# Kernel tuning notes

Hardware: AMD Instinct MI355X
Metric: run time of the kernel (lower is better)

## Reference

```python
import jax, jax.numpy as jnp
import numpy as np

H, D, RPE_DIM, LAYERS = 8, 64, 64, 3
GAMMA = 0.999  # fixed decay (use_decay=True, requires_grad=False)
EPS = 1e-8

def simple_rmsnorm(x):
    # SimpleRMSNorm: x / (||x||_2 * d^{-1/2} + eps), no learned scale
    rms = jnp.sqrt(jnp.sum(x * x, axis=-1, keepdims=True)) * (x.shape[-1] ** -0.5)
    return x / (rms + EPS)

def rpe_transform(idx, pos_proj_w, pos_proj_b, layer_ws, layer_bs, out_w, out_b):
    # idx: (n, 1) -> (H, n, D)
    x = idx @ pos_proj_w + pos_proj_b            # (n, RPE_DIM)
    for i in range(LAYERS):                       # residual=False -> sequential
        x = jax.nn.relu(simple_rmsnorm(x)) @ layer_ws[i] + layer_bs[i]
    x = jax.nn.relu(simple_rmsnorm(x)) @ out_w + out_b   # (n, H*D)
    n = x.shape[0]
    return x.reshape(n, H, D).transpose(1, 0, 2)  # (H, n, D)

def setup_inputs() -> dict:
    key = jax.random.key(0)
    ks = jax.random.split(key, 6)
    b, n = 8, 4096
    s = RPE_DIM ** -0.5
    return {
        "x": jax.random.normal(ks[0], (b, H, n, D), jnp.float32),
        "pos_proj_w": jax.random.normal(ks[1], (1, RPE_DIM), jnp.float32),
        "pos_proj_b": jnp.zeros((RPE_DIM,), jnp.float32),
        "layer_ws": jax.random.normal(ks[2], (LAYERS, RPE_DIM, RPE_DIM), jnp.float32) * s,
        "layer_bs": jnp.zeros((LAYERS, RPE_DIM), jnp.float32),
        "out_w": jax.random.normal(ks[3], (RPE_DIM, H * D), jnp.float32) * s,
        "out_b": jnp.zeros((H * D,), jnp.float32),
    }

def reference(x, pos_proj_w, pos_proj_b, layer_ws, layer_bs, out_w, out_b):
    b, h, n, d = x.shape
    _rpe = lambda idx: rpe_transform(idx, pos_proj_w, pos_proj_b, layer_ws, layer_bs, out_w, out_b)
    # relative-position kernel values (par_type=1: raw integer offsets)
    zero = _rpe(jnp.zeros((1, 1), x.dtype))                       # (H, 1, D)
    pos_idx = jnp.arange(1, n, dtype=x.dtype).reshape(n - 1, 1)   # 1..n-1
    pos = _rpe(pos_idx)                                           # (H, n-1, D)
    neg = _rpe(-pos_idx[::-1])                                    # -(n-1)..-1
    # fixed exponential decay gamma^|offset|
    coef = jnp.arange(1, n, dtype=x.dtype).reshape(1, n - 1, 1)
    gamma = jnp.full((h, 1, d), GAMMA, x.dtype) ** coef           # (H, n-1, D)
    pos = gamma * pos
    neg = gamma[:, ::-1, :] * neg
    # act_type='none' -> identity activation on a
    a = jnp.concatenate([zero, pos, zero, neg], axis=1)           # (H, 2n, D)
    # circular conv of length 2n realizes the Toeplitz matvec
    y = jnp.fft.rfft(x, n=2 * n, axis=-2)                         # (b,H,n+1?,D) complex
    v = jnp.fft.rfft(a, n=2 * n, axis=-2)[None]                   # (1,H,.,D)
    out = jnp.fft.irfft(v * y, n=2 * n, axis=-2)[:, :, :n, :]
    return out
```

## Files before the change

### kernel.cpp

```cpp
#include <hip/hip_runtime.h>
#include <math.h>

#define NF 8192

__device__ __forceinline__ int phys(int e) { return e ^ (((e >> 4) & 7) << 1); }

__device__ __forceinline__ float2 cmul(float2 a, float2 b) {
    return make_float2(a.x*b.x - a.y*b.y, a.x*b.y + a.y*b.x);
}
__device__ __forceinline__ float2 cmulc(float2 a, float2 b) {
    return make_float2(a.x*b.x + a.y*b.y, a.y*b.x - a.x*b.y);
}
__device__ __forceinline__ float2 cadd(float2 a, float2 b){ return make_float2(a.x+b.x, a.y+b.y); }
__device__ __forceinline__ float2 csub(float2 a, float2 b){ return make_float2(a.x-b.x, a.y-b.y); }
__device__ __forceinline__ float2 mnegi(float2 a){ return make_float2(a.y, -a.x); }
__device__ __forceinline__ float2 mposi(float2 a){ return make_float2(-a.y, a.x); }
#define RSQ2 0.70710678118654752f
__device__ __forceinline__ float2 mw81 (float2 a){ return make_float2( RSQ2*(a.x+a.y),  RSQ2*(a.y-a.x)); }
__device__ __forceinline__ float2 mw83 (float2 a){ return make_float2( RSQ2*(a.y-a.x), -RSQ2*(a.x+a.y)); }
__device__ __forceinline__ float2 mw81c(float2 a){ return make_float2( RSQ2*(a.x-a.y),  RSQ2*(a.x+a.y)); }
__device__ __forceinline__ float2 mw83c(float2 a){ return make_float2(-RSQ2*(a.x+a.y),  RSQ2*(a.x-a.y)); }

#define C16_1 0.92387953251128674f
#define S16_1 0.38268343236508978f
#define C16_2 0.70710678118654752f

__device__ __forceinline__ float2 twbase(int ts) {
    float fa = (float)ts * (1.0f/8192.0f);
    return make_float2(__builtin_amdgcn_cosf(fa), -__builtin_amdgcn_sinf(fa));
}

__device__ __forceinline__ void dif8_core(float2& v0, float2& v1, float2& v2, float2& v3,
                                          float2& v4, float2& v5, float2& v6, float2& v7) {
    float2 t;
    t = csub(v0, v4); v0 = cadd(v0, v4); v4 = t;
    t = csub(v1, v5); v1 = cadd(v1, v5); v5 = mw81(t);
    t = csub(v2, v6); v2 = cadd(v2, v6); v6 = mnegi(t);
    t = csub(v3, v7); v3 = cadd(v3, v7); v7 = mw83(t);
    t = csub(v0, v2); v0 = cadd(v0, v2); v2 = t;
    t = csub(v1, v3); v1 = cadd(v1, v3); v3 = mnegi(t);
    t = csub(v4, v6); v4 = cadd(v4, v6); v6 = t;
    t = csub(v5, v7); v5 = cadd(v5, v7); v7 = mnegi(t);
    t = csub(v0, v1); v0 = cadd(v0, v1); v1 = t;
    t = csub(v2, v3); v2 = cadd(v2, v3); v3 = t;
    t = csub(v4, v5); v4 = cadd(v4, v5); v5 = t;
    t = csub(v6, v7); v6 = cadd(v6, v7); v7 = t;
}

__device__ __forceinline__ void dit8_core(float2& v0, float2& v1, float2& v2, float2& v3,
                                          float2& v4, float2& v5, float2& v6, float2& v7) {
    float2 t;
    t = csub(v0, v1); v0 = cadd(v0, v1); v1 = t;
    t = csub(v2, v3); v2 = cadd(v2, v3); v3 = t;
    t = csub(v4, v5); v4 = cadd(v4, v5); v5 = t;
    t = csub(v6, v7); v6 = cadd(v6, v7); v7 = t;
    t = v2;        v2 = csub(v0, t); v0 = cadd(v0, t);
    t = mposi(v3); v3 = csub(v1, t); v1 = cadd(v1, t);
    t = v6;        v6 = csub(v4, t); v4 = cadd(v4, t);
    t = mposi(v7); v7 = csub(v5, t); v5 = cadd(v5, t);
    t = v4;        v4 = csub(v0, t); v0 = cadd(v0, t);
    t = mw81c(v5); v5 = csub(v1, t); v1 = cadd(v1, t);
    t = mposi(v6); v6 = csub(v2, t); v2 = cadd(v2, t);
    t = mw83c(v7); v7 = csub(v3, t); v3 = cadd(v3, t);
}

#define TW_POWERS(ts) \
    float2 w1 = twbase(ts); \
    float2 w2 = cmul(w1, w1); \
    float2 w3 = cmul(w2, w1); \
    float2 w4 = cmul(w2, w2); \
    float2 w5 = cmul(w3, w2); \
    float2 w6 = cmul(w3, w3); \
    float2 w7 = cmul(w4, w3);

template<int M, int LM>
__device__ __forceinline__ void fwd8_lds(float2* Z, int tid) {
    #pragma unroll
    for (int q = 0; q < 2; ++q) {
        int beta = tid + q*512;
        int i    = beta & (M-1);
        int base = ((beta >> LM) << (LM+3)) + i;
        float2 v0 = Z[phys(base        )];
        float2 v1 = Z[phys(base + 1*M)];
        float2 v2 = Z[phys(base + 2*M)];
        float2 v3 = Z[phys(base + 3*M)];
        float2 v4 = Z[phys(base + 4*M)];
        float2 v5 = Z[phys(base + 5*M)];
        float2 v6 = Z[phys(base + 6*M)];
        float2 v7 = Z[phys(base + 7*M)];
        dif8_core(v0,v1,v2,v3,v4,v5,v6,v7);
        TW_POWERS((NF >> (LM+3)) * i)
        Z[phys(base        )] = v0;
        Z[phys(base + 4*M)] = cmul(v1, w4);
        Z[phys(base + 2*M)] = cmul(v2, w2);
        Z[phys(base + 6*M)] = cmul(v3, w6);
        Z[phys(base + 1*M)] = cmul(v4, w1);
        Z[phys(base + 5*M)] = cmul(v5, w5);
        Z[phys(base + 3*M)] = cmul(v6, w3);
        Z[phys(base + 7*M)] = cmul(v7, w7);
    }
}

template<int M, int LM>
__device__ __forceinline__ void inv8_lds(float2* Z, int tid) {
    #pragma unroll
    for (int q = 0; q < 2; ++q) {
        int beta = tid + q*512;
        int i    = beta & (M-1);
        int base = ((beta >> LM) << (LM+3)) + i;
        TW_POWERS((NF >> (LM+3)) * i)
        float2 v0 = Z[phys(base        )];
        float2 v1 = cmulc(Z[phys(base + 4*M)], w4);
        float2 v2 = cmulc(Z[phys(base + 2*M)], w2);
        float2 v3 = cmulc(Z[phys(base + 6*M)], w6);
        float2 v4 = cmulc(Z[phys(base + 1*M)], w1);
        float2 v5 = cmulc(Z[phys(base + 5*M)], w5);
        float2 v6 = cmulc(Z[phys(base + 3*M)], w3);
        float2 v7 = cmulc(Z[phys(base + 7*M)], w7);
        dit8_core(v0,v1,v2,v3,v4,v5,v6,v7);
        Z[phys(base        )] = v0;
        Z[phys(base + 1*M)] = v1;
        Z[phys(base + 2*M)] = v2;
        Z[phys(base + 3*M)] = v3;
        Z[phys(base + 4*M)] = v4;
        Z[phys(base + 5*M)] = v5;
        Z[phys(base + 6*M)] = v6;
        Z[phys(base + 7*M)] = v7;
    }
}

__device__ __forceinline__ void fft8192_conv(float2* Z, int tid, const float4* __restrict__ A4,
                                             const float2 (&vin)[8], float2 (&vout)[8])
{
    #pragma unroll
    for (int q = 0; q < 2; ++q) {
        int i = tid + q*512;
        float2 v0 = vin[q*4+0];
        float2 v1 = vin[q*4+1];
        float2 v2 = vin[q*4+2];
        float2 v3 = vin[q*4+3];
        float2 v4 = v0;
        float2 v5 = mw81(v1);
        float2 v6 = mnegi(v2);
        float2 v7 = mw83(v3);
        float2 t;
        t = csub(v0, v2); v0 = cadd(v0, v2); v2 = t;
        t = csub(v1, v3); v1 = cadd(v1, v3); v3 = mnegi(t);
        t = csub(v4, v6); v4 = cadd(v4, v6); v6 = t;
        t = csub(v5, v7); v5 = cadd(v5, v7); v7 = mnegi(t);
        t = csub(v0, v1); v0 = cadd(v0, v1); v1 = t;
        t = csub(v2, v3); v2 = cadd(v2, v3); v3 = t;
        t = csub(v4, v5); v4 = cadd(v4, v5); v5 = t;
        t = csub(v6, v7); v6 = cadd(v6, v7); v7 = t;
        TW_POWERS(i)
        Z[phys(i        )] = v0;
        Z[phys(i + 4096)] = cmul(v1, w4);
        Z[phys(i + 2048)] = cmul(v2, w2);
        Z[phys(i + 6144)] = cmul(v3, w6);
        Z[phys(i + 1024)] = cmul(v4, w1);
        Z[phys(i + 5120)] = cmul(v5, w5);
        Z[phys(i + 3072)] = cmul(v6, w3);
        Z[phys(i + 7168)] = cmul(v7, w7);
    }
    __syncthreads();
    fwd8_lds<128, 7>(Z, tid);  __syncthreads();
    fwd8_lds<16,  4>(Z, tid);  __syncthreads();

    {
        int c = tid, sw4 = c & 7;
        float4* Z4 = reinterpret_cast<float4*>(Z);
        float2 z[16];
        #pragma unroll
        for (int j = 0; j < 8; ++j) {
            float4 wv = Z4[c*8 + (j ^ sw4)];
            z[2*j]   = make_float2(wv.x, wv.y);
            z[2*j+1] = make_float2(wv.z, wv.w);
        }
        dif8_core(z[0],z[2],z[4],z[6],z[8],z[10],z[12],z[14]);
        dif8_core(z[1],z[3],z[5],z[7],z[9],z[11],z[13],z[15]);
        #define P4K(k, ZE, ZO, WR, WI) { \
            float2 w = make_float2((WR)*(ZO).x - (WI)*(ZO).y, (WR)*(ZO).y + (WI)*(ZO).x); \
            float2 pp = cadd(ZE, w), rr = csub(ZE, w); \
            float4 av = A4[(k)*512 + c]; \
            pp = cmul(pp, make_float2(av.x, av.y)); \
            rr = cmul(rr, make_float2(av.z, av.w)); \
            ZE = cadd(pp, rr); \
            ZO = csub(pp, rr); }
        { float2 pp = cadd(z[0], z[1]), rr = csub(z[0], z[1]);
          float4 av = A4[0*512 + c];
          pp = cmul(pp, make_float2(av.x, av.y));
          rr = cmul(rr, make_float2(av.z, av.w));
          z[0] = cadd(pp, rr); z[1] = csub(pp, rr); }
        P4K(1, z[8],  z[9],   C16_1, -S16_1)
        P4K(2, z[4],  z[5],   C16_2, -C16_2)
        P4K(3, z[12], z[13],  S16_1, -C16_1)
        { float2 w = mnegi(z[3]);
          float2 pp = cadd(z[2], w), rr = csub(z[2], w);
          float4 av = A4[4*512 + c];
          pp = cmul(pp, make_float2(av.x, av.y));
          rr = cmul(rr, make_float2(av.z, av.w));
          z[2] = cadd(pp, rr); z[3] = csub(pp, rr); }
        P4K(5, z[10], z[11], -S16_1, -C16_1)
        P4K(6, z[6],  z[7],  -C16_2, -C16_2)
        P4K(7, z[14], z[15], -C16_1, -S16_1)
        #undef P4K
        z[3]  = mposi(z[3]);
        z[5]  = cmul(z[5],  make_float2( C16_2,  C16_2));
        z[7]  = cmul(z[7],  make_float2(-C16_2,  C16_2));
        z[9]  = cmul(z[9],  make_float2( C16_1,  S16_1));
        z[11] = cmul(z[11], make_float2(-S16_1,  C16_1));
        z[13] = cmul(z[13], make_float2( S16_1,  C16_1));
        z[15] = cmul(z[15], make_float2(-C16_1,  S16_1));
        dit8_core(z[0],z[2],z[4],z[6],z[8],z[10],z[12],z[14]);
        dit8_core(z[1],z[3],z[5],z[7],z[9],z[11],z[13],z[15]);
        #pragma unroll
        for (int j = 0; j < 8; ++j)
            Z4[c*8 + (j ^ sw4)] = make_float4(z[2*j].x, z[2*j].y, z[2*j+1].x, z[2*j+1].y);
    }
    __syncthreads();
    inv8_lds<16,  4>(Z, tid);  __syncthreads();
    inv8_lds<128, 7>(Z, tid);  __syncthreads();

    #pragma unroll
    for (int q = 0; q < 2; ++q) {
        int i = tid + q*512;
        TW_POWERS(i)
        float2 v0 = Z[phys(i        )];
        float2 v1 = cmulc(Z[phys(i + 4096)], w4);
        float2 v2 = cmulc(Z[phys(i + 2048)], w2);
        float2 v3 = cmulc(Z[phys(i + 6144)], w6);
        float2 v4 = cmulc(Z[phys(i + 1024)], w1);
        float2 v5 = cmulc(Z[phys(i + 5120)], w5);
        float2 v6 = cmulc(Z[phys(i + 3072)], w3);
        float2 v7 = cmulc(Z[phys(i + 7168)], w7);
        float2 t;
        t = csub(v0, v1); v0 = cadd(v0, v1); v1 = t;
        t = csub(v2, v3); v2 = cadd(v2, v3); v3 = t;
        t = csub(v4, v5); v4 = cadd(v4, v5); v5 = t;
        t = csub(v6, v7); v6 = cadd(v6, v7); v7 = t;
        t = v2;        v2 = csub(v0, t); v0 = cadd(v0, t);
        t = mposi(v3); v3 = csub(v1, t); v1 = cadd(v1, t);
        t = v6;        v6 = csub(v4, t); v4 = cadd(v4, t);
        t = mposi(v7); v7 = csub(v5, t); v5 = cadd(v5, t);
        vout[q*4+0] = cadd(v0, v4);
        vout[q*4+1] = cadd(v1, mw81c(v5));
        vout[q*4+2] = cadd(v2, mposi(v6));
        vout[q*4+3] = cadd(v3, mw83c(v7));
    }
}


__global__ __launch_bounds__(512) void rpe_kernel(
    const float* __restrict__ pw,  const float* __restrict__ pb,
    const float* __restrict__ lws, const float* __restrict__ lbs,
    const float* __restrict__ ow,  const float* __restrict__ ob,
    float* __restrict__ a_buf)
{
    __shared__ float sW2[3][32][64][2];
    __shared__ float sWo2[32][64][2];
    __shared__ float sB[3][64];
    __shared__ float sPW[64], sPB[64];
    __shared__ float sAct[8][2][64];
    int tid = threadIdx.x;
    for (int idx = tid; idx < 3*64*64; idx += 512) {
        int L = idx >> 12, rem = idx & 4095, k = rem >> 6, c = rem & 63;
        sW2[L][k >> 1][c][k & 1] = lws[idx];
    }
    if (tid < 192) ((float*)sB)[tid] = lbs[tid];
    if (tid < 64) { sPW[tid] = pw[tid]; sPB[tid] = pb[tid]; }
    __syncthreads();

    int wv = tid >> 6, lane = tid & 63;
    int e0 = blockIdx.x * 16 + wv * 2;
    float xv[2], dec[2];
    #pragma unroll
    for (int s = 0; s < 2; ++s) {
        int e = e0 + s;
        float p = (e == 4096) ? 0.f : ((e < 4096) ? (float)e : (float)(e - 8192));
        int m = (e < 4096) ? e : (8192 - e);
        if (e == 4096) m = 0;
        dec[s] = exp2f(-0.0014434309482562475f * (float)m);
        xv[s] = fmaf(p, sPW[lane], sPB[lane]);
    }

    #pragma unroll
    for (int L = 0; L < 3; ++L) {
        #pragma unroll
        for (int s = 0; s < 2; ++s) {
            float v = xv[s];
            float ss = v * v;
            #pragma unroll
            for (int o = 1; o < 64; o <<= 1) ss += __shfl_xor(ss, o);
            sAct[wv][s][lane] = fmaxf(v / (sqrtf(ss) * 0.125f + 1e-8f), 0.f);
            float y = sB[L][lane];
            const float2* ap = reinterpret_cast<const float2*>(sAct[wv][s]);
            const float2* wp = reinterpret_cast<const float2*>(sW2[L]);
            #pragma unroll
            for (int kk = 0; kk < 32; ++kk) {
                float2 a2 = ap[kk];
                float2 ww = wp[kk*64 + lane];
                y = fmaf(a2.x, ww.x, y);
                y = fmaf(a2.y, ww.y, y);
            }
            xv[s] = y;
        }
    }
    #pragma unroll
    for (int s = 0; s < 2; ++s) {
        float v = xv[s];
        float ss = v * v;
        #pragma unroll
        for (int o = 1; o < 64; o <<= 1) ss += __shfl_xor(ss, o);
        sAct[wv][s][lane] = fmaxf(v / (sqrtf(ss) * 0.125f + 1e-8f), 0.f);
    }
    for (int qq = 0; qq < 8; ++qq) {
        __syncthreads();
        for (int idx = tid; idx < 4096; idx += 512) {
            int k = idx >> 6, c = idx & 63;
            sWo2[k >> 1][c][k & 1] = ow[(size_t)k*512 + qq*64 + c];
        }
        __syncthreads();
        #pragma unroll
        for (int s = 0; s < 2; ++s) {
            float y = ob[qq*64 + lane];
            const float2* ap = reinterpret_cast<const float2*>(sAct[wv][s]);
            const float2* wp = reinterpret_cast<const float2*>(sWo2);
            #pragma unroll
            for (int kk = 0; kk < 32; ++kk) {
                float2 a2 = ap[kk];
                float2 ww = wp[kk*64 + lane];
                y = fmaf(a2.x, ww.x, y);
                y = fmaf(a2.y, ww.y, y);
            }
            a_buf[(size_t)(qq*64 + lane)*NF + (e0 + s)] = y * dec[s];
        }
    }
}

__global__ __launch_bounds__(512, 4) void afft_kernel(
    const float* __restrict__ a_buf, float2* __restrict__ Afft)
{
    __shared__ __align__(16) float2 Z[NF];
    int cc = blockIdx.x, tid = threadIdx.x;
    const float* col = a_buf + (size_t)cc * NF;
    #pragma unroll
    for (int q = 0; q < 2; ++q) {
        int i = tid + q*512;
        float2 v0 = make_float2(col[i       ], 0.f);
        float2 v1 = make_float2(col[i + 1024], 0.f);
        float2 v2 = make_float2(col[i + 2048], 0.f);
        float2 v3 = make_float2(col[i + 3072], 0.f);
        float2 v4 = make_float2(col[i + 4096], 0.f);
        float2 v5 = make_float2(col[i + 5120], 0.f);
        float2 v6 = make_float2(col[i + 6144], 0.f);
        float2 v7 = make_float2(col[i + 7168], 0.f);
        dif8_core(v0,v1,v2,v3,v4,v5,v6,v7);
        TW_POWERS(i)
        Z[phys(i        )] = v0;
        Z[phys(i + 4096)] = cmul(v1, w4);
        Z[phys(i + 2048)] = cmul(v2, w2);
        Z[phys(i + 6144)] = cmul(v3, w6);
        Z[phys(i + 1024)] = cmul(v4, w1);
        Z[phys(i + 5120)] = cmul(v5, w5);
        Z[phys(i + 3072)] = cmul(v6, w3);
        Z[phys(i + 7168)] = cmul(v7, w7);
    }
    __syncthreads();
    fwd8_lds<128, 7>(Z, tid);  __syncthreads();
    fwd8_lds<16,  4>(Z, tid);  __syncthreads();
    {
        int c = tid, sw4 = c & 7;
        float4* Z4 = reinterpret_cast<float4*>(Z);
        float4* oc4 = reinterpret_cast<float4*>(Afft + (size_t)cc * NF);
        float2 z[16];
        #pragma unroll
        for (int j = 0; j < 8; ++j) {
            float4 wv = Z4[c*8 + (j ^ sw4)];
            z[2*j]   = make_float2(wv.x, wv.y);
            z[2*j+1] = make_float2(wv.z, wv.w);
        }
        dif8_core(z[0],z[2],z[4],z[6],z[8],z[10],z[12],z[14]);
        dif8_core(z[1],z[3],z[5],z[7],z[9],z[11],z[13],z[15]);
        #define A4K(k, ZE, ZO, WR, WI) { \
            float2 w = make_float2((WR)*(ZO).x - (WI)*(ZO).y, (WR)*(ZO).y + (WI)*(ZO).x); \
            float2 pp = cadd(ZE, w), rr = csub(ZE, w); \
            oc4[(k)*512 + c] = make_float4(pp.x, pp.y, rr.x, rr.y); }
        { float2 pp = cadd(z[0], z[1]), rr = csub(z[0], z[1]);
          oc4[0*512 + c] = make_float4(pp.x, pp.y, rr.x, rr.y); }
        A4K(1, z[8],  z[9],   C16_1, -S16_1)
        A4K(2, z[4],  z[5],   C16_2, -C16_2)
        A4K(3, z[12], z[13],  S16_1, -C16_1)
        { float2 w = mnegi(z[3]);
          float2 pp = cadd(z[2], w), rr = csub(z[2], w);
          oc4[4*512 + c] = make_float4(pp.x, pp.y, rr.x, rr.y); }
        A4K(5, z[10], z[11], -S16_1, -C16_1)
        A4K(6, z[6],  z[7],  -C16_2, -C16_2)
        A4K(7, z[14], z[15], -C16_1, -S16_1)
        #undef A4K
    }
}

__global__ __launch_bounds__(512, 4) void conv_kernel(
    const float* __restrict__ x, const float2* __restrict__ Afft,
    float* __restrict__ out)
{
    __shared__ __align__(16) float2 Z[NF];
    int blk = blockIdx.x;
    int c8 = blk & 7, r = blk >> 3;
    int dp = ((c8 & 1) << 4) | (r & 15);
    int h  = (((r >> 4) & 3) << 1) | ((c8 >> 1) & 1);
    int bp = (((r >> 6) & 1) << 1) | ((c8 >> 2) & 1);
    int d  = dp * 2;
    int tid = threadIdx.x;
    size_t base0 = ((size_t)((bp*2 + 0)*8 + h) * 4096) * 64 + d;
    size_t base1 = ((size_t)((bp*2 + 1)*8 + h) * 4096) * 64 + d;

    float2 inA[8], inB[8];
    #pragma unroll
    for (int q = 0; q < 2; ++q) {
        #pragma unroll
        for (int l = 0; l < 4; ++l) {
            int p = tid + q*512 + l*1024;
            float2 f0 = *reinterpret_cast<const float2*>(&x[base0 + (size_t)p*64]);
            float2 f1 = *reinterpret_cast<const float2*>(&x[base1 + (size_t)p*64]);
            inA[q*4+l] = make_float2(f0.x, f1.x);
            inB[q*4+l] = make_float2(f0.y, f1.y);
        }
    }

    const float4* A4a = reinterpret_cast<const float4*>(Afft + (size_t)(h*64 + d    )*NF);
    const float4* A4b = reinterpret_cast<const float4*>(Afft + (size_t)(h*64 + d + 1)*NF);
    float2 outA[8], outB[8];
    fft8192_conv(Z, tid, A4a, inA, outA);
    __syncthreads();
    fft8192_conv(Z, tid, A4b, inB, outB);

    const float sc = 1.0f/8192.0f;
    #pragma unroll
    for (int q = 0; q < 2; ++q) {
        #pragma unroll
        for (int l = 0; l < 4; ++l) {
            int p = tid + q*512 + l*1024;
            float2 yA = outA[q*4+l], yB = outB[q*4+l];
            *reinterpret_cast<float2*>(&out[base0 + (size_t)p*64]) = make_float2(yA.x * sc, yB.x * sc);
            *reinterpret_cast<float2*>(&out[base1 + (size_t)p*64]) = make_float2(yA.y * sc, yB.y * sc);
        }
    }
}

extern "C" void kernel_launch(void* const* d_in, const int* in_sizes, int n_in,
                              void* d_out, int out_size, void* d_ws, size_t ws_size,
                              hipStream_t stream) {
    const float* x   = (const float*)d_in[0];
    const float* pw  = (const float*)d_in[1];
    const float* pb  = (const float*)d_in[2];
    const float* lws = (const float*)d_in[3];
    const float* lbs = (const float*)d_in[4];
    const float* ow  = (const float*)d_in[5];
    const float* ob  = (const float*)d_in[6];
    float* out = (float*)d_out;
    char* ws = (char*)d_ws;
    float*  a_buf = (float*)ws;
    float2* Afft  = (float2*)(ws + (size_t)512*NF*4);

    rpe_kernel<<<512, 512, 0, stream>>>(pw, pb, lws, lbs, ow, ob, a_buf);
    afft_kernel<<<512, 512, 0, stream>>>(a_buf, Afft);
    conv_kernel<<<1024, 512, 0, stream>>>(x, Afft, out);
}
```

Baseline: 616.1 us.

## Pack two adjacent real channels into one complex FFT with Hermitian split

```diff
diff --git a/kernel.cpp b/kernel.cpp
--- a/kernel.cpp
+++ b/kernel.cpp
@@ -129,16 +129,177 @@
     }
 }
 
-__device__ __forceinline__ void fft8192_conv(float2* Z, int tid, const float4* __restrict__ A4,
-                                             const float2 (&vin)[8], float2 (&vout)[8])
+
+__global__ __launch_bounds__(512) void rpe_kernel(
+    const float* __restrict__ pw,  const float* __restrict__ pb,
+    const float* __restrict__ lws, const float* __restrict__ lbs,
+    const float* __restrict__ ow,  const float* __restrict__ ob,
+    float* __restrict__ a_buf)
 {
+    __shared__ float sW2[3][32][64][2];
+    __shared__ float sWo2[32][64][2];
+    __shared__ float sB[3][64];
+    __shared__ float sPW[64], sPB[64];
+    __shared__ float sAct[8][2][64];
+    int tid = threadIdx.x;
+    for (int idx = tid; idx < 3*64*64; idx += 512) {
+        int L = idx >> 12, rem = idx & 4095, k = rem >> 6, c = rem & 63;
+        sW2[L][k >> 1][c][k & 1] = lws[idx];
+    }
+    if (tid < 192) ((float*)sB)[tid] = lbs[tid];
+    if (tid < 64) { sPW[tid] = pw[tid]; sPB[tid] = pb[tid]; }
+    __syncthreads();
+
+    int wv = tid >> 6, lane = tid & 63;
+    int e0 = blockIdx.x * 16 + wv * 2;
+    float xv[2], dec[2];
+    #pragma unroll
+    for (int s = 0; s < 2; ++s) {
+        int e = e0 + s;
+        float p = (e == 4096) ? 0.f : ((e < 4096) ? (float)e : (float)(e - 8192));
+        int m = (e < 4096) ? e : (8192 - e);
+        if (e == 4096) m = 0;
+        dec[s] = exp2f(-0.0014434309482562475f * (float)m);
+        xv[s] = fmaf(p, sPW[lane], sPB[lane]);
+    }
+
+    #pragma unroll
+    for (int L = 0; L < 3; ++L) {
+        #pragma unroll
+        for (int s = 0; s < 2; ++s) {
+            float v = xv[s];
+            float ss = v * v;
+            #pragma unroll
+            for (int o = 1; o < 64; o <<= 1) ss += __shfl_xor(ss, o);
+            sAct[wv][s][lane] = fmaxf(v / (sqrtf(ss) * 0.125f + 1e-8f), 0.f);
+            float y = sB[L][lane];
+            const float2* ap = reinterpret_cast<const float2*>(sAct[wv][s]);
+            const float2* wp = reinterpret_cast<const float2*>(sW2[L]);
+            #pragma unroll
+            for (int kk = 0; kk < 32; ++kk) {
+                float2 a2 = ap[kk];
+                float2 ww = wp[kk*64 + lane];
+                y = fmaf(a2.x, ww.x, y);
+                y = fmaf(a2.y, ww.y, y);
+            }
+            xv[s] = y;
+        }
+    }
+    #pragma unroll
+    for (int s = 0; s < 2; ++s) {
+        float v = xv[s];
+        float ss = v * v;
+        #pragma unroll
+        for (int o = 1; o < 64; o <<= 1) ss += __shfl_xor(ss, o);
+        sAct[wv][s][lane] = fmaxf(v / (sqrtf(ss) * 0.125f + 1e-8f), 0.f);
+    }
+    for (int qq = 0; qq < 8; ++qq) {
+        __syncthreads();
+        for (int idx = tid; idx < 4096; idx += 512) {
+            int k = idx >> 6, c = idx & 63;
+            sWo2[k >> 1][c][k & 1] = ow[(size_t)k*512 + qq*64 + c];
+        }
+        __syncthreads();
+        #pragma unroll
+        for (int s = 0; s < 2; ++s) {
+            float y = ob[qq*64 + lane];
+            const float2* ap = reinterpret_cast<const float2*>(sAct[wv][s]);
+            const float2* wp = reinterpret_cast<const float2*>(sWo2);
+            #pragma unroll
+            for (int kk = 0; kk < 32; ++kk) {
+                float2 a2 = ap[kk];
+                float2 ww = wp[kk*64 + lane];
+                y = fmaf(a2.x, ww.x, y);
+                y = fmaf(a2.y, ww.y, y);
+            }
+            a_buf[(size_t)(qq*64 + lane)*NF + (e0 + s)] = y * dec[s];
+        }
+    }
+}
+
+__global__ __launch_bounds__(512, 4) void afft_kernel(
+    const float* __restrict__ a_buf, float2* __restrict__ Afft)
+{
+    __shared__ __align__(16) float2 Z[NF];
+    int cc = blockIdx.x, tid = threadIdx.x;
+    const float* col = a_buf + (size_t)cc * NF;
     #pragma unroll
     for (int q = 0; q < 2; ++q) {
         int i = tid + q*512;
-        float2 v0 = vin[q*4+0];
-        float2 v1 = vin[q*4+1];
-        float2 v2 = vin[q*4+2];
-        float2 v3 = vin[q*4+3];
+        float2 v0 = make_float2(col[i       ], 0.f);
+        float2 v1 = make_float2(col[i + 1024], 0.f);
+        float2 v2 = make_float2(col[i + 2048], 0.f);
+        float2 v3 = make_float2(col[i + 3072], 0.f);
+        float2 v4 = make_float2(col[i + 4096], 0.f);
+        float2 v5 = make_float2(col[i + 5120], 0.f);
+        float2 v6 = make_float2(col[i + 6144], 0.f);
+        float2 v7 = make_float2(col[i + 7168], 0.f);
+        dif8_core(v0,v1,v2,v3,v4,v5,v6,v7);
+        TW_POWERS(i)
+        Z[phys(i        )] = v0;
+        Z[phys(i + 4096)] = cmul(v1, w4);
+        Z[phys(i + 2048)] = cmul(v2, w2);
+        Z[phys(i + 6144)] = cmul(v3, w6);
+        Z[phys(i + 1024)] = cmul(v4, w1);
+        Z[phys(i + 5120)] = cmul(v5, w5);
+        Z[phys(i + 3072)] = cmul(v6, w3);
+        Z[phys(i + 7168)] = cmul(v7, w7);
+    }
+    __syncthreads();
+    fwd8_lds<128, 7>(Z, tid);  __syncthreads();
+    fwd8_lds<16,  4>(Z, tid);  __syncthreads();
+    {
+        int c = tid, sw4 = c & 7;
+        float4* Z4 = reinterpret_cast<float4*>(Z);
+        float4* oc4 = reinterpret_cast<float4*>(Afft + (size_t)cc * NF);
+        float2 z[16];
+        #pragma unroll
+        for (int j = 0; j < 8; ++j) {
+            float4 wv = Z4[c*8 + (j ^ sw4)];
+            z[2*j]   = make_float2(wv.x, wv.y);
+            z[2*j+1] = make_float2(wv.z, wv.w);
+        }
+        dif8_core(z[0],z[2],z[4],z[6],z[8],z[10],z[12],z[14]);
+        dif8_core(z[1],z[3],z[5],z[7],z[9],z[11],z[13],z[15]);
+        #define A4K(k, ZE, ZO, WR, WI) { \
+            float2 w = make_float2((WR)*(ZO).x - (WI)*(ZO).y, (WR)*(ZO).y + (WI)*(ZO).x); \
+            float2 pp = cadd(ZE, w), rr = csub(ZE, w); \
+            oc4[(k)*512 + c] = make_float4(pp.x, pp.y, rr.x, rr.y); }
+        { float2 pp = cadd(z[0], z[1]), rr = csub(z[0], z[1]);
+          oc4[0*512 + c] = make_float4(pp.x, pp.y, rr.x, rr.y); }
+        A4K(1, z[8],  z[9],   C16_1, -S16_1)
+        A4K(2, z[4],  z[5],   C16_2, -C16_2)
+        A4K(3, z[12], z[13],  S16_1, -C16_1)
+        { float2 w = mnegi(z[3]);
+          float2 pp = cadd(z[2], w), rr = csub(z[2], w);
+          oc4[4*512 + c] = make_float4(pp.x, pp.y, rr.x, rr.y); }
+        A4K(5, z[10], z[11], -S16_1, -C16_1)
+        A4K(6, z[6],  z[7],  -C16_2, -C16_2)
+        A4K(7, z[14], z[15], -C16_1, -S16_1)
+        #undef A4K
+    }
+}
+
+__global__ __launch_bounds__(512, 4) void conv_kernel(
+    const float* __restrict__ x, const float2* __restrict__ Afft,
+    float* __restrict__ out)
+{
+    __shared__ __align__(16) float2 Z[NF];
+    int blk = blockIdx.x;
+    int b   = blk & 7;
+    int q   = blk >> 3;
+    int h   = q >> 5;
+    int dp  = q & 31;
+    int tid = threadIdx.x;
+    size_t base = ((size_t)(b*8 + h) * 4096) * 64 + 2*dp;
+
+    #pragma unroll
+    for (int qq = 0; qq < 2; ++qq) {
+        int i = tid + qq*512;
+        float2 v0 = *reinterpret_cast<const float2*>(&x[base + (size_t)(i       )*64]);
+        float2 v1 = *reinterpret_cast<const float2*>(&x[base + (size_t)(i + 1024)*64]);
+        float2 v2 = *reinterpret_cast<const float2*>(&x[base + (size_t)(i + 2048)*64]);
+        float2 v3 = *reinterpret_cast<const float2*>(&x[base + (size_t)(i + 3072)*64]);
         float2 v4 = v0;
         float2 v5 = mw81(v1);
         float2 v6 = mnegi(v2);
@@ -168,62 +329,108 @@
 
     {
         int c = tid, sw4 = c & 7;
+        int l  = (c >> 6) | (((c >> 3) & 7) << 3) | ((c & 7) << 6);
+        int lp = (512 - l) & 511;
+        int cp = ((lp & 7) << 6) | (((lp >> 3) & 7) << 3) | (lp >> 6);
+        int swp = cp & 7;
+        bool l0 = (l == 0);
         float4* Z4 = reinterpret_cast<float4*>(Z);
-        float2 z[16];
+        const float4* A4a = reinterpret_cast<const float4*>(Afft + (size_t)(h*64 + 2*dp    )*NF);
+        const float4* A4b = reinterpret_cast<const float4*>(Afft + (size_t)(h*64 + 2*dp + 1)*NF);
+
+        float2 zz[16];
         #pragma unroll
         for (int j = 0; j < 8; ++j) {
             float4 wv = Z4[c*8 + (j ^ sw4)];
-            z[2*j]   = make_float2(wv.x, wv.y);
-            z[2*j+1] = make_float2(wv.z, wv.w);
-        }
-        dif8_core(z[0],z[2],z[4],z[6],z[8],z[10],z[12],z[14]);
-        dif8_core(z[1],z[3],z[5],z[7],z[9],z[11],z[13],z[15]);
-        #define P4K(k, ZE, ZO, WR, WI) { \
-            float2 w = make_float2((WR)*(ZO).x - (WI)*(ZO).y, (WR)*(ZO).y + (WI)*(ZO).x); \
-            float2 pp = cadd(ZE, w), rr = csub(ZE, w); \
-            float4 av = A4[(k)*512 + c]; \
-            pp = cmul(pp, make_float2(av.x, av.y)); \
-            rr = cmul(rr, make_float2(av.z, av.w)); \
-            ZE = cadd(pp, rr); \
-            ZO = csub(pp, rr); }
-        { float2 pp = cadd(z[0], z[1]), rr = csub(z[0], z[1]);
-          float4 av = A4[0*512 + c];
-          pp = cmul(pp, make_float2(av.x, av.y));
-          rr = cmul(rr, make_float2(av.z, av.w));
-          z[0] = cadd(pp, rr); z[1] = csub(pp, rr); }
-        P4K(1, z[8],  z[9],   C16_1, -S16_1)
-        P4K(2, z[4],  z[5],   C16_2, -C16_2)
-        P4K(3, z[12], z[13],  S16_1, -C16_1)
-        { float2 w = mnegi(z[3]);
-          float2 pp = cadd(z[2], w), rr = csub(z[2], w);
-          float4 av = A4[4*512 + c];
-          pp = cmul(pp, make_float2(av.x, av.y));
-          rr = cmul(rr, make_float2(av.z, av.w));
-          z[2] = cadd(pp, rr); z[3] = csub(pp, rr); }
-        P4K(5, z[10], z[11], -S16_1, -C16_1)
-        P4K(6, z[6],  z[7],  -C16_2, -C16_2)
-        P4K(7, z[14], z[15], -C16_1, -S16_1)
-        #undef P4K
-        z[3]  = mposi(z[3]);
-        z[5]  = cmul(z[5],  make_float2( C16_2,  C16_2));
-        z[7]  = cmul(z[7],  make_float2(-C16_2,  C16_2));
-        z[9]  = cmul(z[9],  make_float2( C16_1,  S16_1));
-        z[11] = cmul(z[11], make_float2(-S16_1,  C16_1));
-        z[13] = cmul(z[13], make_float2( S16_1,  C16_1));
-        z[15] = cmul(z[15], make_float2(-C16_1,  S16_1));
-        dit8_core(z[0],z[2],z[4],z[6],z[8],z[10],z[12],z[14]);
-        dit8_core(z[1],z[3],z[5],z[7],z[9],z[11],z[13],z[15]);
+            zz[2*j]   = make_float2(wv.x, wv.y);
+            zz[2*j+1] = make_float2(wv.z, wv.w);
+        }
+        dif8_core(zz[0],zz[2],zz[4],zz[6],zz[8],zz[10],zz[12],zz[14]);
+        dif8_core(zz[1],zz[3],zz[5],zz[7],zz[9],zz[11],zz[13],zz[15]);
+        float2 S[16];
+        #define SPLIT(kk, JE, WR, WI) { \
+            float2 E = zz[2*(JE)], O = zz[2*(JE)+1]; \
+            float2 wo = make_float2((WR)*O.x - (WI)*O.y, (WR)*O.y + (WI)*O.x); \
+            S[kk] = cadd(E, wo); S[(kk)+8] = csub(E, wo); }
+        SPLIT(0, 0,  1.0f,   0.0f)
+        SPLIT(1, 4,  C16_1, -S16_1)
+        SPLIT(2, 2,  C16_2, -C16_2)
+        SPLIT(3, 6,  S16_1, -C16_1)
+        SPLIT(4, 1,  0.0f,  -1.0f)
+        SPLIT(5, 5, -S16_1, -C16_1)
+        SPLIT(6, 3, -C16_2, -C16_2)
+        SPLIT(7, 7, -C16_1, -S16_1)
+        #undef SPLIT
+        {
+            const int rev3[8] = {0,4,2,6,1,5,3,7};
+            #pragma unroll
+            for (int j = 0; j < 8; ++j) {
+                int m = rev3[j];
+                Z4[c*8 + (j ^ sw4)] = make_float4(S[m].x, S[m].y, S[m+8].x, S[m+8].y);
+            }
+        }
+        __syncthreads();
+        float2 Sp[16];
+        {
+            const int rev3[8] = {0,4,2,6,1,5,3,7};
+            #pragma unroll
+            for (int j = 0; j < 8; ++j) {
+                float4 wv = Z4[cp*8 + (j ^ swp)];
+                int m = rev3[j];
+                Sp[m]   = make_float2(wv.x, wv.y);
+                Sp[m+8] = make_float2(wv.z, wv.w);
+            }
+        }
+        float2 Yv[16];
+        #define YPAIR(kk, IA0, IB0, IA8, IB8) { \
+            float4 aa = A4a[(kk)*512 + c]; \
+            float4 ab = A4b[(kk)*512 + c]; \
+            { float2 P = l0 ? Sp[IA0] : Sp[IB0]; \
+              float2 E = make_float2(0.5f*(S[kk].x + P.x),  0.5f*(S[kk].y - P.y)); \
+              float2 O = make_float2(0.5f*(S[kk].y + P.y), -0.5f*(S[kk].x - P.x)); \
+              Yv[kk] = cadd(cmul(E, make_float2(aa.x, aa.y)), mposi(cmul(O, make_float2(ab.x, ab.y)))); } \
+            { float2 P = l0 ? Sp[IA8] : Sp[IB8]; \
+              float2 E = make_float2(0.5f*(S[(kk)+8].x + P.x),  0.5f*(S[(kk)+8].y - P.y)); \
+              float2 O = make_float2(0.5f*(S[(kk)+8].y + P.y), -0.5f*(S[(kk)+8].x - P.x)); \
+              Yv[(kk)+8] = cadd(cmul(E, make_float2(aa.z, aa.w)), mposi(cmul(O, make_float2(ab.z, ab.w)))); } }
+        YPAIR(0,  0, 15, 8, 7)
+        YPAIR(1, 15, 14, 7, 6)
+        YPAIR(2, 14, 13, 6, 5)
+        YPAIR(3, 13, 12, 5, 4)
+        YPAIR(4, 12, 11, 4, 3)
+        YPAIR(5, 11, 10, 3, 2)
+        YPAIR(6, 10,  9, 2, 1)
+        YPAIR(7,  9,  8, 1, 0)
+        #undef YPAIR
+        #define GPAIR(kk, JE, WRC, WIC) { \
+            float2 GE = cadd(Yv[kk], Yv[(kk)+8]); \
+            float2 GO = csub(Yv[kk], Yv[(kk)+8]); \
+            zz[2*(JE)]   = GE; \
+            zz[2*(JE)+1] = make_float2((WRC)*GO.x - (WIC)*GO.y, (WRC)*GO.y + (WIC)*GO.x); }
+        GPAIR(0, 0,  1.0f,  0.0f)
+        GPAIR(1, 4,  C16_1, S16_1)
+        GPAIR(2, 2,  C16_2, C16_2)
+        GPAIR(3, 6,  S16_1, C16_1)
+        GPAIR(4, 1,  0.0f,  1.0f)
+        GPAIR(5, 5, -S16_1, C16_1)
+        GPAIR(6, 3, -C16_2, C16_2)
+        GPAIR(7, 7, -C16_1, S16_1)
+        #undef GPAIR
+        dit8_core(zz[0],zz[2],zz[4],zz[6],zz[8],zz[10],zz[12],zz[14]);
+        dit8_core(zz[1],zz[3],zz[5],zz[7],zz[9],zz[11],zz[13],zz[15]);
+        __syncthreads();
         #pragma unroll
         for (int j = 0; j < 8; ++j)
-            Z4[c*8 + (j ^ sw4)] = make_float4(z[2*j].x, z[2*j].y, z[2*j+1].x, z[2*j+1].y);
+            Z4[c*8 + (j ^ sw4)] = make_float4(zz[2*j].x, zz[2*j].y, zz[2*j+1].x, zz[2*j+1].y);
     }
     __syncthreads();
     inv8_lds<16,  4>(Z, tid);  __syncthreads();
     inv8_lds<128, 7>(Z, tid);  __syncthreads();
 
-    #pragma unroll
-    for (int q = 0; q < 2; ++q) {
-        int i = tid + q*512;
+    const float sc = 1.0f/8192.0f;
+    #pragma unroll
+    for (int qq = 0; qq < 2; ++qq) {
+        int i = tid + qq*512;
         TW_POWERS(i)
         float2 v0 = Z[phys(i        )];
         float2 v1 = cmulc(Z[phys(i + 4096)], w4);
@@ -242,209 +449,14 @@
         t = mposi(v3); v3 = csub(v1, t); v1 = cadd(v1, t);
         t = v6;        v6 = csub(v4, t); v4 = cadd(v4, t);
         t = mposi(v7); v7 = csub(v5, t); v5 = cadd(v5, t);
-        vout[q*4+0] = cadd(v0, v4);
-        vout[q*4+1] = cadd(v1, mw81c(v5));
-        vout[q*4+2] = cadd(v2, mposi(v6));
-        vout[q*4+3] = cadd(v3, mw83c(v7));
-    }
-}
-
-
-__global__ __launch_bounds__(512) void rpe_kernel(
-    const float* __restrict__ pw,  const float* __restrict__ pb,
-    const float* __restrict__ lws, const float* __restrict__ lbs,
-    const float* __restrict__ ow,  const float* __restrict__ ob,
-    float* __restrict__ a_buf)
-{
-    __shared__ float sW2[3][32][64][2];
-    __shared__ float sWo2[32][64][2];
-    __shared__ float sB[3][64];
-    __shared__ float sPW[64], sPB[64];
-    __shared__ float sAct[8][2][64];
-    int tid = threadIdx.x;
-    for (int idx = tid; idx < 3*64*64; idx += 512) {
-        int L = idx >> 12, rem = idx & 4095, k = rem >> 6, c = rem & 63;
-        sW2[L][k >> 1][c][k & 1] = lws[idx];
-    }
-    if (tid < 192) ((float*)sB)[tid] = lbs[tid];
-    if (tid < 64) { sPW[tid] = pw[tid]; sPB[tid] = pb[tid]; }
-    __syncthreads();
-
-    int wv = tid >> 6, lane = tid & 63;
-    int e0 = blockIdx.x * 16 + wv * 2;
-    float xv[2], dec[2];
-    #pragma unroll
-    for (int s = 0; s < 2; ++s) {
-        int e = e0 + s;
-        float p = (e == 4096) ? 0.f : ((e < 4096) ? (float)e : (float)(e - 8192));
-        int m = (e < 4096) ? e : (8192 - e);
-        if (e == 4096) m = 0;
-        dec[s] = exp2f(-0.0014434309482562475f * (float)m);
-        xv[s] = fmaf(p, sPW[lane], sPB[lane]);
-    }
-
-    #pragma unroll
-    for (int L = 0; L < 3; ++L) {
-        #pragma unroll
-        for (int s = 0; s < 2; ++s) {
-            float v = xv[s];
-            float ss = v * v;
-            #pragma unroll
-            for (int o = 1; o < 64; o <<= 1) ss += __shfl_xor(ss, o);
-            sAct[wv][s][lane] = fmaxf(v / (sqrtf(ss) * 0.125f + 1e-8f), 0.f);
-            float y = sB[L][lane];
-            const float2* ap = reinterpret_cast<const float2*>(sAct[wv][s]);
-            const float2* wp = reinterpret_cast<const float2*>(sW2[L]);
-            #pragma unroll
-            for (int kk = 0; kk < 32; ++kk) {
-                float2 a2 = ap[kk];
-                float2 ww = wp[kk*64 + lane];
-                y = fmaf(a2.x, ww.x, y);
-                y = fmaf(a2.y, ww.y, y);
-            }
-            xv[s] = y;
-        }
-    }
-    #pragma unroll
-    for (int s = 0; s < 2; ++s) {
-        float v = xv[s];
-        float ss = v * v;
-        #pragma unroll
-        for (int o = 1; o < 64; o <<= 1) ss += __shfl_xor(ss, o);
-        sAct[wv][s][lane] = fmaxf(v / (sqrtf(ss) * 0.125f + 1e-8f), 0.f);
-    }
-    for (int qq = 0; qq < 8; ++qq) {
-        __syncthreads();
-        for (int idx = tid; idx < 4096; idx += 512) {
-            int k = idx >> 6, c = idx & 63;
-            sWo2[k >> 1][c][k & 1] = ow[(size_t)k*512 + qq*64 + c];
-        }
-        __syncthreads();
-        #pragma unroll
-        for (int s = 0; s < 2; ++s) {
-            float y = ob[qq*64 + lane];
-            const float2* ap = reinterpret_cast<const float2*>(sAct[wv][s]);
-            const float2* wp = reinterpret_cast<const float2*>(sWo2);
-            #pragma unroll
-            for (int kk = 0; kk < 32; ++kk) {
-                float2 a2 = ap[kk];
-                float2 ww = wp[kk*64 + lane];
-                y = fmaf(a2.x, ww.x, y);
-                y = fmaf(a2.y, ww.y, y);
-            }
-            a_buf[(size_t)(qq*64 + lane)*NF + (e0 + s)] = y * dec[s];
-        }
-    }
-}
-
-__global__ __launch_bounds__(512, 4) void afft_kernel(
-    const float* __restrict__ a_buf, float2* __restrict__ Afft)
-{
-    __shared__ __align__(16) float2 Z[NF];
-    int cc = blockIdx.x, tid = threadIdx.x;
-    const float* col = a_buf + (size_t)cc * NF;
-    #pragma unroll
-    for (int q = 0; q < 2; ++q) {
-        int i = tid + q*512;
-        float2 v0 = make_float2(col[i       ], 0.f);
-        float2 v1 = make_float2(col[i + 1024], 0.f);
-        float2 v2 = make_float2(col[i + 2048], 0.f);
-        float2 v3 = make_float2(col[i + 3072], 0.f);
-        float2 v4 = make_float2(col[i + 4096], 0.f);
-        float2 v5 = make_float2(col[i + 5120], 0.f);
-        float2 v6 = make_float2(col[i + 6144], 0.f);
-        float2 v7 = make_float2(col[i + 7168], 0.f);
-        dif8_core(v0,v1,v2,v3,v4,v5,v6,v7);
-        TW_POWERS(i)
-        Z[phys(i        )] = v0;
-        Z[phys(i + 4096)] = cmul(v1, w4);
-        Z[phys(i + 2048)] = cmul(v2, w2);
-        Z[phys(i + 6144)] = cmul(v3, w6);
-        Z[phys(i + 1024)] = cmul(v4, w1);
-        Z[phys(i + 5120)] = cmul(v5, w5);
-        Z[phys(i + 3072)] = cmul(v6, w3);
-        Z[phys(i + 7168)] = cmul(v7, w7);
-    }
-    __syncthreads();
-    fwd8_lds<128, 7>(Z, tid);  __syncthreads();
-    fwd8_lds<16,  4>(Z, tid);  __syncthreads();
-    {
-        int c = tid, sw4 = c & 7;
-        float4* Z4 = reinterpret_cast<float4*>(Z);
-        float4* oc4 = reinterpret_cast<float4*>(Afft + (size_t)cc * NF);
-        float2 z[16];
-        #pragma unroll
-        for (int j = 0; j < 8; ++j) {
-            float4 wv = Z4[c*8 + (j ^ sw4)];
-            z[2*j]   = make_float2(wv.x, wv.y);
-            z[2*j+1] = make_float2(wv.z, wv.w);
-        }
-        dif8_core(z[0],z[2],z[4],z[6],z[8],z[10],z[12],z[14]);
-        dif8_core(z[1],z[3],z[5],z[7],z[9],z[11],z[13],z[15]);
-        #define A4K(k, ZE, ZO, WR, WI) { \
-            float2 w = make_float2((WR)*(ZO).x - (WI)*(ZO).y, (WR)*(ZO).y + (WI)*(ZO).x); \
-            float2 pp = cadd(ZE, w), rr = csub(ZE, w); \
-            oc4[(k)*512 + c] = make_float4(pp.x, pp.y, rr.x, rr.y); }
-        { float2 pp = cadd(z[0], z[1]), rr = csub(z[0], z[1]);
-          oc4[0*512 + c] = make_float4(pp.x, pp.y, rr.x, rr.y); }
-        A4K(1, z[8],  z[9],   C16_1, -S16_1)
-        A4K(2, z[4],  z[5],   C16_2, -C16_2)
-        A4K(3, z[12], z[13],  S16_1, -C16_1)
-        { float2 w = mnegi(z[3]);
-          float2 pp = cadd(z[2], w), rr = csub(z[2], w);
-          oc4[4*512 + c] = make_float4(pp.x, pp.y, rr.x, rr.y); }
-        A4K(5, z[10], z[11], -S16_1, -C16_1)
-        A4K(6, z[6],  z[7],  -C16_2, -C16_2)
-        A4K(7, z[14], z[15], -C16_1, -S16_1)
-        #undef A4K
-    }
-}
-
-__global__ __launch_bounds__(512, 4) void conv_kernel(
-    const float* __restrict__ x, const float2* __restrict__ Afft,
-    float* __restrict__ out)
-{
-    __shared__ __align__(16) float2 Z[NF];
-    int blk = blockIdx.x;
-    int c8 = blk & 7, r = blk >> 3;
-    int dp = ((c8 & 1) << 4) | (r & 15);
-    int h  = (((r >> 4) & 3) << 1) | ((c8 >> 1) & 1);
-    int bp = (((r >> 6) & 1) << 1) | ((c8 >> 2) & 1);
-    int d  = dp * 2;
-    int tid = threadIdx.x;
-    size_t base0 = ((size_t)((bp*2 + 0)*8 + h) * 4096) * 64 + d;
-    size_t base1 = ((size_t)((bp*2 + 1)*8 + h) * 4096) * 64 + d;
-
-    float2 inA[8], inB[8];
-    #pragma unroll
-    for (int q = 0; q < 2; ++q) {
-        #pragma unroll
-        for (int l = 0; l < 4; ++l) {
-            int p = tid + q*512 + l*1024;
-            float2 f0 = *reinterpret_cast<const float2*>(&x[base0 + (size_t)p*64]);
-            float2 f1 = *reinterpret_cast<const float2*>(&x[base1 + (size_t)p*64]);
-            inA[q*4+l] = make_float2(f0.x, f1.x);
-            inB[q*4+l] = make_float2(f0.y, f1.y);
-        }
-    }
-
-    const float4* A4a = reinterpret_cast<const float4*>(Afft + (size_t)(h*64 + d    )*NF);
-    const float4* A4b = reinterpret_cast<const float4*>(Afft + (size_t)(h*64 + d + 1)*NF);
-    float2 outA[8], outB[8];
-    fft8192_conv(Z, tid, A4a, inA, outA);
-    __syncthreads();
-    fft8192_conv(Z, tid, A4b, inB, outB);
-
-    const float sc = 1.0f/8192.0f;
-    #pragma unroll
-    for (int q = 0; q < 2; ++q) {
-        #pragma unroll
-        for (int l = 0; l < 4; ++l) {
-            int p = tid + q*512 + l*1024;
-            float2 yA = outA[q*4+l], yB = outB[q*4+l];
-            *reinterpret_cast<float2*>(&out[base0 + (size_t)p*64]) = make_float2(yA.x * sc, yB.x * sc);
-            *reinterpret_cast<float2*>(&out[base1 + (size_t)p*64]) = make_float2(yA.y * sc, yB.y * sc);
-        }
+        v0 = cadd(v0, v4);
+        v1 = cadd(v1, mw81c(v5));
+        v2 = cadd(v2, mposi(v6));
+        v3 = cadd(v3, mw83c(v7));
+        *reinterpret_cast<float2*>(&out[base + (size_t)(i       )*64]) = make_float2(v0.x*sc, v0.y*sc);
+        *reinterpret_cast<float2*>(&out[base + (size_t)(i + 1024)*64]) = make_float2(v1.x*sc, v1.y*sc);
+        *reinterpret_cast<float2*>(&out[base + (size_t)(i + 2048)*64]) = make_float2(v2.x*sc, v2.y*sc);
+        *reinterpret_cast<float2*>(&out[base + (size_t)(i + 3072)*64]) = make_float2(v3.x*sc, v3.y*sc);
     }
 }
 
@@ -465,5 +477,5 @@
 
     rpe_kernel<<<512, 512, 0, stream>>>(pw, pb, lws, lbs, ow, ob, a_buf);
     afft_kernel<<<512, 512, 0, stream>>>(a_buf, Afft);
-    conv_kernel<<<1024, 512, 0, stream>>>(x, Afft, out);
-}
+    conv_kernel<<<2048, 512, 0, stream>>>(x, Afft, out);
+}
```

After: 495.5 us. -19.6%, faster.
